# Kernel optimization log

Measured on AMD Instinct MI355X. Metric: run time of the kernel, lower is better.

## Reference

```python
import jax, jax.numpy as jnp
import numpy as np

KH, KW = 3, 3
STRIDE = (1, 1)


def setup_inputs() -> dict:
    key = jax.random.key(0)
    k1, k2, k3 = jax.random.split(key, 3)
    N, C, H, W = 16, 128, 64, 64
    O = 128
    x = jax.random.normal(k1, (N, C, H, W), dtype=jnp.float32)
    # Flat weight layout [O, C*KH*KW], matching torch reshape of [O,C,KH,KW]
    weight = jax.random.normal(k2, (O, C * KH * KW), dtype=jnp.float32) * 0.02
    bias = jax.random.normal(k3, (O, 1), dtype=jnp.float32) * 0.02
    return {"x": x, "weight": weight, "bias": bias}


def reference(x, weight, bias):
    O = weight.shape[0]
    C = x.shape[1]
    # [O, C*KH*KW] -> [O, C, KH, KW]; flattening order (C major, then kh, kw)
    # matches the module's unfold/permute im2col layout.
    w4 = weight.reshape(O, C, KH, KW)
    out = jax.lax.conv_general_dilated(
        x, w4,
        window_strides=STRIDE,
        padding='VALID',
        dimension_numbers=('NCHW', 'OIHW', 'NCHW'),
    )
    return out + bias.reshape(1, O, 1, 1)
```

## Files before the change

### kernel.cpp

```cpp
#include <hip/hip_runtime.h>
#include <stdint.h>

#define AS_G __attribute__((address_space(1)))
#define AS_L __attribute__((address_space(3)))

typedef __bf16 bf16x8 __attribute__((ext_vector_type(8)));
typedef float  f32x4  __attribute__((ext_vector_type(4)));

static constexpr int NIMG = 16, CIN = 128, H = 64, W = 64, OCH = 128;
static constexpr int HO = 62, WO = 62;
static constexpr int PIX = HO * WO;
static constexpr int M_TOT = NIMG * PIX;
static constexpr int K_TOT = CIN * 9;
static constexpr int BM = 64, BK = 64;
static constexpr int KSTEPS = K_TOT / BK;

__device__ __forceinline__ unsigned short f2bf(float f) {
    union { float f; uint32_t u; } v; v.f = f;
    uint32_t u = v.u;
    return (unsigned short)((u + 0x7FFFu + ((u >> 16) & 1u)) >> 16);
}

__global__ __launch_bounds__(256) void xpose_kernel(const float* __restrict__ x,
                                                    unsigned short* __restrict__ xt) {
    __shared__ float lds[CIN][W + 4];
    const int n   = blockIdx.x >> 6;
    const int h   = blockIdx.x & 63;
    const int tid = threadIdx.x;
    {
        const int c  = tid >> 1;
        const int w0 = (tid & 1) * 32;
        const float* src = x + (((size_t)(n * CIN + c) * H + h) * W + w0);
        #pragma unroll
        for (int j = 0; j < 8; ++j) {
            float4 v = *reinterpret_cast<const float4*>(src + j * 4);
            *reinterpret_cast<float4*>(&lds[c][w0 + j * 4]) = v;
        }
    }
    __syncthreads();
    {
        const int w  = tid >> 2;
        const int c0 = (tid & 3) * 32;
        unsigned short* dst = xt + (((size_t)(n * H + h) * W + w) * CIN + c0);
        uint32_t pk[16];
        #pragma unroll
        for (int j = 0; j < 16; ++j) {
            uint32_t lo = f2bf(lds[c0 + 2 * j][w]);
            uint32_t hi = f2bf(lds[c0 + 2 * j + 1][w]);
            pk[j] = lo | (hi << 16);
        }
        #pragma unroll
        for (int j = 0; j < 4; ++j) {
            *reinterpret_cast<uint4*>(dst + j * 8) =
                make_uint4(pk[4 * j], pk[4 * j + 1], pk[4 * j + 2], pk[4 * j + 3]);
        }
    }
}

__global__ __launch_bounds__(256) void wprep_kernel(const float* __restrict__ wsrc,
                                                    unsigned short* __restrict__ bpd) {
    int tid = blockIdx.x * 256 + threadIdx.x;
    if (tid >= OCH * K_TOT) return;
    int o  = tid / K_TOT;
    int kp = tid - o * K_TOT;
    int t  = kp >> 7;
    int c  = kp & 127;
    bpd[tid] = f2bf(wsrc[o * K_TOT + c * 9 + t]);
}

__global__ __launch_bounds__(256) void gemm_kernel(const unsigned short* __restrict__ xt,
                                                   const unsigned short* __restrict__ bp,
                                                   const float* __restrict__ bias,
                                                   float* __restrict__ out) {
    __shared__ alignas(16) unsigned short As[BM * BK];
    __shared__ alignas(16) unsigned short Bs[OCH * BK];
    const int tid  = threadIdx.x;
    const int wv   = tid >> 6;
    const int lane = tid & 63;
    const int m0   = blockIdx.x * BM;

    const int csel = ((lane & 7) ^ (lane >> 3)) * 8;
    int aBase[2], bBase[4];
    #pragma unroll
    for (int i = 0; i < 2; ++i) {
        int row = (wv * 2 + i) * 8 + (lane >> 3);
        int m = m0 + row;
        int n  = m / PIX;
        int r  = m - n * PIX;
        int y  = r / WO;
        int xx = r - y * WO;
        aBase[i] = ((n * H + y) * W + xx) * CIN;
    }
    #pragma unroll
    for (int i = 0; i < 4; ++i) {
        int row = (wv * 4 + i) * 8 + (lane >> 3);
        bBase[i] = row * K_TOT;
    }

    const int wr = wv >> 1, wc = wv & 1;
    const int lr = lane & 15, lq = lane >> 4;
    const int aRow = (wr * 32 + lr) * 128;
    const int bRow = (wc * 64 + lr) * 128;
    int colx[2];
    #pragma unroll
    for (int ks = 0; ks < 2; ++ks)
        colx[ks] = (ks * 64 + lq * 16) ^ ((lane & 7) << 4);

    f32x4 acc[2][4];
    #pragma unroll
    for (int a = 0; a < 2; ++a)
        #pragma unroll
        for (int b = 0; b < 4; ++b)
            acc[a][b] = (f32x4){0.f, 0.f, 0.f, 0.f};

    const char* AsB = (const char*)As;
    const char* BsB = (const char*)Bs;

    for (int step = 0; step < KSTEPS; ++step) {
        const int t  = step >> 1;
        const int c0 = (step & 1) * 64;
        const int tapoff = (t / 3) * (W * CIN) + (t % 3) * CIN + c0;
        const int kb = step * BK;
        #pragma unroll
        for (int i = 0; i < 2; ++i)
            __builtin_amdgcn_global_load_lds(
                (AS_G unsigned int*)(xt + aBase[i] + tapoff + csel),
                (AS_L unsigned int*)((char*)As + (wv * 2 + i) * 1024),
                16, 0, 0);
        #pragma unroll
        for (int i = 0; i < 4; ++i)
            __builtin_amdgcn_global_load_lds(
                (AS_G unsigned int*)(bp + bBase[i] + kb + csel),
                (AS_L unsigned int*)((char*)Bs + (wv * 4 + i) * 1024),
                16, 0, 0);
        __syncthreads();
        #pragma unroll
        for (int ks = 0; ks < 2; ++ks) {
            bf16x8 af[2], bfr[4];
            #pragma unroll
            for (int mi = 0; mi < 2; ++mi)
                af[mi] = *(const bf16x8*)(AsB + aRow + mi * 2048 + colx[ks]);
            #pragma unroll
            for (int ni = 0; ni < 4; ++ni)
                bfr[ni] = *(const bf16x8*)(BsB + bRow + ni * 2048 + colx[ks]);
            #pragma unroll
            for (int mi = 0; mi < 2; ++mi)
                #pragma unroll
                for (int ni = 0; ni < 4; ++ni)
                    acc[mi][ni] = __builtin_amdgcn_mfma_f32_16x16x32_bf16(
                        bfr[ni], af[mi], acc[mi][ni], 0, 0, 0);
        }
        __syncthreads();
    }

    f32x4 bv[4];
    #pragma unroll
    for (int ni = 0; ni < 4; ++ni)
        bv[ni] = *(const f32x4*)(bias + wc * 64 + ni * 16 + lq * 4);
    #pragma unroll
    for (int mi = 0; mi < 2; ++mi) {
        int m = m0 + wr * 32 + mi * 16 + lr;
        int n  = m / PIX;
        int r  = m - n * PIX;
        int y  = r / WO;
        int xx = r - y * WO;
        float* ob = out + (size_t)n * OCH * PIX + y * WO + xx;
        #pragma unroll
        for (int ni = 0; ni < 4; ++ni)
            #pragma unroll
            for (int j = 0; j < 4; ++j) {
                int o = wc * 64 + ni * 16 + lq * 4 + j;
                ob[(size_t)o * PIX] = acc[mi][ni][j] + bv[ni][j];
            }
    }
}

extern "C" void kernel_launch(void* const* d_in, const int* in_sizes, int n_in,
                              void* d_out, int out_size, void* d_ws, size_t ws_size,
                              hipStream_t stream) {
    const float* x    = (const float*)d_in[0];
    const float* wsrc = (const float*)d_in[1];
    const float* bias = (const float*)d_in[2];
    float* out = (float*)d_out;
    unsigned short* xt = (unsigned short*)d_ws;
    unsigned short* bp = xt + (size_t)NIMG * H * W * CIN;
    xpose_kernel<<<dim3(NIMG * H), dim3(256), 0, stream>>>(x, xt);
    wprep_kernel<<<dim3((OCH * K_TOT + 255) / 256), dim3(256), 0, stream>>>(wsrc, bp);
    gemm_kernel<<<dim3(M_TOT / BM), dim3(256), 0, stream>>>(xt, bp, bias, out);
}
```

Before: 46.40 us.

## Double-buffer GEMM LDS staging and merge input/weight prep kernels

The GEMM main loop now uses two LDS buffers and issues the global-to-LDS loads for the next K step before computing the current one, so load latency overlaps the MFMA work. It keeps one barrier per iteration instead of two. The transpose and weight-conversion kernels are merged into a single launch, removing one kernel launch. LDS usage per block doubles, which may lower occupancy.

```diff
diff --git a/kernel.cpp b/kernel.cpp
--- a/kernel.cpp
+++ b/kernel.cpp
@@ -14,6 +14,7 @@
 static constexpr int K_TOT = CIN * 9;
 static constexpr int BM = 64, BK = 64;
 static constexpr int KSTEPS = K_TOT / BK;
+static constexpr int BUFB = 24576;
 
 __device__ __forceinline__ unsigned short f2bf(float f) {
     union { float f; uint32_t u; } v; v.f = f;
@@ -21,59 +22,60 @@
     return (unsigned short)((u + 0x7FFFu + ((u >> 16) & 1u)) >> 16);
 }
 
-__global__ __launch_bounds__(256) void xpose_kernel(const float* __restrict__ x,
-                                                    unsigned short* __restrict__ xt) {
+__global__ __launch_bounds__(256) void prep_kernel(const float* __restrict__ x,
+                                                   const float* __restrict__ wsrc,
+                                                   unsigned short* __restrict__ xt,
+                                                   unsigned short* __restrict__ bpd) {
     __shared__ float lds[CIN][W + 4];
-    const int n   = blockIdx.x >> 6;
-    const int h   = blockIdx.x & 63;
-    const int tid = threadIdx.x;
-    {
-        const int c  = tid >> 1;
-        const int w0 = (tid & 1) * 32;
-        const float* src = x + (((size_t)(n * CIN + c) * H + h) * W + w0);
-        #pragma unroll
-        for (int j = 0; j < 8; ++j) {
-            float4 v = *reinterpret_cast<const float4*>(src + j * 4);
-            *reinterpret_cast<float4*>(&lds[c][w0 + j * 4]) = v;
+    if (blockIdx.x < NIMG * H) {
+        const int n   = blockIdx.x >> 6;
+        const int h   = blockIdx.x & 63;
+        const int tid = threadIdx.x;
+        {
+            const int c  = tid >> 1;
+            const int w0 = (tid & 1) * 32;
+            const float* src = x + (((size_t)(n * CIN + c) * H + h) * W + w0);
+            #pragma unroll
+            for (int j = 0; j < 8; ++j) {
+                float4 v = *reinterpret_cast<const float4*>(src + j * 4);
+                *reinterpret_cast<float4*>(&lds[c][w0 + j * 4]) = v;
+            }
+        }
+        __syncthreads();
+        {
+            const int w  = tid >> 2;
+            const int c0 = (tid & 3) * 32;
+            unsigned short* dst = xt + (((size_t)(n * H + h) * W + w) * CIN + c0);
+            uint32_t pk[16];
+            #pragma unroll
+            for (int j = 0; j < 16; ++j) {
+                uint32_t lo = f2bf(lds[c0 + 2 * j][w]);
+                uint32_t hi = f2bf(lds[c0 + 2 * j + 1][w]);
+                pk[j] = lo | (hi << 16);
+            }
+            #pragma unroll
+            for (int j = 0; j < 4; ++j) {
+                *reinterpret_cast<uint4*>(dst + j * 8) =
+                    make_uint4(pk[4 * j], pk[4 * j + 1], pk[4 * j + 2], pk[4 * j + 3]);
+            }
+        }
+    } else {
+        int tid = (blockIdx.x - NIMG * H) * 256 + threadIdx.x;
+        if (tid < OCH * K_TOT) {
+            int o  = tid / K_TOT;
+            int kp = tid - o * K_TOT;
+            int t  = kp >> 7;
+            int c  = kp & 127;
+            bpd[tid] = f2bf(wsrc[o * K_TOT + c * 9 + t]);
         }
     }
-    __syncthreads();
-    {
-        const int w  = tid >> 2;
-        const int c0 = (tid & 3) * 32;
-        unsigned short* dst = xt + (((size_t)(n * H + h) * W + w) * CIN + c0);
-        uint32_t pk[16];
-        #pragma unroll
-        for (int j = 0; j < 16; ++j) {
-            uint32_t lo = f2bf(lds[c0 + 2 * j][w]);
-            uint32_t hi = f2bf(lds[c0 + 2 * j + 1][w]);
-            pk[j] = lo | (hi << 16);
-        }
-        #pragma unroll
-        for (int j = 0; j < 4; ++j) {
-            *reinterpret_cast<uint4*>(dst + j * 8) =
-                make_uint4(pk[4 * j], pk[4 * j + 1], pk[4 * j + 2], pk[4 * j + 3]);
-        }
-    }
-}
-
-__global__ __launch_bounds__(256) void wprep_kernel(const float* __restrict__ wsrc,
-                                                    unsigned short* __restrict__ bpd) {
-    int tid = blockIdx.x * 256 + threadIdx.x;
-    if (tid >= OCH * K_TOT) return;
-    int o  = tid / K_TOT;
-    int kp = tid - o * K_TOT;
-    int t  = kp >> 7;
-    int c  = kp & 127;
-    bpd[tid] = f2bf(wsrc[o * K_TOT + c * 9 + t]);
 }
 
 __global__ __launch_bounds__(256) void gemm_kernel(const unsigned short* __restrict__ xt,
                                                    const unsigned short* __restrict__ bp,
                                                    const float* __restrict__ bias,
                                                    float* __restrict__ out) {
-    __shared__ alignas(16) unsigned short As[BM * BK];
-    __shared__ alignas(16) unsigned short Bs[OCH * BK];
+    __shared__ alignas(16) char lds[2 * BUFB];
     const int tid  = threadIdx.x;
     const int wv   = tid >> 6;
     const int lane = tid & 63;
@@ -92,10 +94,26 @@
         aBase[i] = ((n * H + y) * W + xx) * CIN;
     }
     #pragma unroll
-    for (int i = 0; i < 4; ++i) {
-        int row = (wv * 4 + i) * 8 + (lane >> 3);
-        bBase[i] = row * K_TOT;
-    }
+    for (int i = 0; i < 4; ++i)
+        bBase[i] = ((wv * 4 + i) * 8 + (lane >> 3)) * K_TOT;
+
+    auto stage = [&](int buf, int step) {
+        const int t  = step >> 1;
+        const int c0 = (step & 1) * 64;
+        const int tapoff = (t / 3) * (W * CIN) + (t % 3) * CIN + c0;
+        const int kb = step * BK;
+        char* dst = lds + buf * BUFB;
+        #pragma unroll
+        for (int i = 0; i < 2; ++i)
+            __builtin_amdgcn_global_load_lds(
+                (AS_G unsigned int*)(xt + aBase[i] + tapoff + csel),
+                (AS_L unsigned int*)(dst + (wv * 2 + i) * 1024), 16, 0, 0);
+        #pragma unroll
+        for (int i = 0; i < 4; ++i)
+            __builtin_amdgcn_global_load_lds(
+                (AS_G unsigned int*)(bp + bBase[i] + kb + csel),
+                (AS_L unsigned int*)(dst + 8192 + (wv * 4 + i) * 1024), 16, 0, 0);
+    };
 
     const int wr = wv >> 1, wc = wv & 1;
     const int lr = lane & 15, lq = lane >> 4;
@@ -113,36 +131,23 @@
         for (int b = 0; b < 4; ++b)
             acc[a][b] = (f32x4){0.f, 0.f, 0.f, 0.f};
 
-    const char* AsB = (const char*)As;
-    const char* BsB = (const char*)Bs;
+    stage(0, 0);
+    __syncthreads();
 
+    #pragma unroll 2
     for (int step = 0; step < KSTEPS; ++step) {
-        const int t  = step >> 1;
-        const int c0 = (step & 1) * 64;
-        const int tapoff = (t / 3) * (W * CIN) + (t % 3) * CIN + c0;
-        const int kb = step * BK;
-        #pragma unroll
-        for (int i = 0; i < 2; ++i)
-            __builtin_amdgcn_global_load_lds(
-                (AS_G unsigned int*)(xt + aBase[i] + tapoff + csel),
-                (AS_L unsigned int*)((char*)As + (wv * 2 + i) * 1024),
-                16, 0, 0);
-        #pragma unroll
-        for (int i = 0; i < 4; ++i)
-            __builtin_amdgcn_global_load_lds(
-                (AS_G unsigned int*)(bp + bBase[i] + kb + csel),
-                (AS_L unsigned int*)((char*)Bs + (wv * 4 + i) * 1024),
-                16, 0, 0);
-        __syncthreads();
+        const int buf = step & 1;
+        if (step + 1 < KSTEPS) stage(buf ^ 1, step + 1);
+        const char* base = lds + buf * BUFB;
         #pragma unroll
         for (int ks = 0; ks < 2; ++ks) {
             bf16x8 af[2], bfr[4];
             #pragma unroll
             for (int mi = 0; mi < 2; ++mi)
-                af[mi] = *(const bf16x8*)(AsB + aRow + mi * 2048 + colx[ks]);
+                af[mi] = *(const bf16x8*)(base + aRow + mi * 2048 + colx[ks]);
             #pragma unroll
             for (int ni = 0; ni < 4; ++ni)
-                bfr[ni] = *(const bf16x8*)(BsB + bRow + ni * 2048 + colx[ks]);
+                bfr[ni] = *(const bf16x8*)(base + 8192 + bRow + ni * 2048 + colx[ks]);
             #pragma unroll
             for (int mi = 0; mi < 2; ++mi)
                 #pragma unroll
@@ -184,7 +189,7 @@
     float* out = (float*)d_out;
     unsigned short* xt = (unsigned short*)d_ws;
     unsigned short* bp = xt + (size_t)NIMG * H * W * CIN;
-    xpose_kernel<<<dim3(NIMG * H), dim3(256), 0, stream>>>(x, xt);
-    wprep_kernel<<<dim3((OCH * K_TOT + 255) / 256), dim3(256), 0, stream>>>(wsrc, bp);
+    prep_kernel<<<dim3(NIMG * H + (OCH * K_TOT + 255) / 256), dim3(256), 0, stream>>>(
+        x, wsrc, xt, bp);
     gemm_kernel<<<dim3(M_TOT / BM), dim3(256), 0, stream>>>(xt, bp, bias, out);
 }
```

Measured after the change: 48.72 us. 5.0% more time.

## Merge prep kernels and remap GEMM workgroups to contiguous XCD chunks

Applied to the files above, without the earlier changes.

Fuses the input-transpose and weight-prep kernels into one launch, with blocks split by block index, to save a kernel launch and its gap. In the GEMM, blockIdx is remapped so that each of the 8 XCDs (blocks are assigned round-robin) handles a contiguous range of M tiles: 121 tiles for the first XCD and 120 for each of the others. The aim is L2 reuse of the overlapping 3x3 input rows between neighbouring tiles on the same XCD. The remap hardcodes the tile count and assumes round-robin XCD dispatch.

```diff
diff --git a/kernel.cpp b/kernel.cpp
--- a/kernel.cpp
+++ b/kernel.cpp
@@ -14,6 +14,7 @@
 static constexpr int K_TOT = CIN * 9;
 static constexpr int BM = 64, BK = 64;
 static constexpr int KSTEPS = K_TOT / BK;
+static constexpr int NWG = M_TOT / BM;
 
 __device__ __forceinline__ unsigned short f2bf(float f) {
     union { float f; uint32_t u; } v; v.f = f;
@@ -21,51 +22,53 @@
     return (unsigned short)((u + 0x7FFFu + ((u >> 16) & 1u)) >> 16);
 }
 
-__global__ __launch_bounds__(256) void xpose_kernel(const float* __restrict__ x,
-                                                    unsigned short* __restrict__ xt) {
+__global__ __launch_bounds__(256) void prep_kernel(const float* __restrict__ x,
+                                                   const float* __restrict__ wsrc,
+                                                   unsigned short* __restrict__ xt,
+                                                   unsigned short* __restrict__ bpd) {
     __shared__ float lds[CIN][W + 4];
-    const int n   = blockIdx.x >> 6;
-    const int h   = blockIdx.x & 63;
-    const int tid = threadIdx.x;
-    {
-        const int c  = tid >> 1;
-        const int w0 = (tid & 1) * 32;
-        const float* src = x + (((size_t)(n * CIN + c) * H + h) * W + w0);
-        #pragma unroll
-        for (int j = 0; j < 8; ++j) {
-            float4 v = *reinterpret_cast<const float4*>(src + j * 4);
-            *reinterpret_cast<float4*>(&lds[c][w0 + j * 4]) = v;
+    if (blockIdx.x < NIMG * H) {
+        const int n   = blockIdx.x >> 6;
+        const int h   = blockIdx.x & 63;
+        const int tid = threadIdx.x;
+        {
+            const int c  = tid >> 1;
+            const int w0 = (tid & 1) * 32;
+            const float* src = x + (((size_t)(n * CIN + c) * H + h) * W + w0);
+            #pragma unroll
+            for (int j = 0; j < 8; ++j) {
+                float4 v = *reinterpret_cast<const float4*>(src + j * 4);
+                *reinterpret_cast<float4*>(&lds[c][w0 + j * 4]) = v;
+            }
+        }
+        __syncthreads();
+        {
+            const int w  = tid >> 2;
+            const int c0 = (tid & 3) * 32;
+            unsigned short* dst = xt + (((size_t)(n * H + h) * W + w) * CIN + c0);
+            uint32_t pk[16];
+            #pragma unroll
+            for (int j = 0; j < 16; ++j) {
+                uint32_t lo = f2bf(lds[c0 + 2 * j][w]);
+                uint32_t hi = f2bf(lds[c0 + 2 * j + 1][w]);
+                pk[j] = lo | (hi << 16);
+            }
+            #pragma unroll
+            for (int j = 0; j < 4; ++j) {
+                *reinterpret_cast<uint4*>(dst + j * 8) =
+                    make_uint4(pk[4 * j], pk[4 * j + 1], pk[4 * j + 2], pk[4 * j + 3]);
+            }
+        }
+    } else {
+        int tid = (blockIdx.x - NIMG * H) * 256 + threadIdx.x;
+        if (tid < OCH * K_TOT) {
+            int o  = tid / K_TOT;
+            int kp = tid - o * K_TOT;
+            int t  = kp >> 7;
+            int c  = kp & 127;
+            bpd[tid] = f2bf(wsrc[o * K_TOT + c * 9 + t]);
         }
     }
-    __syncthreads();
-    {
-        const int w  = tid >> 2;
-        const int c0 = (tid & 3) * 32;
-        unsigned short* dst = xt + (((size_t)(n * H + h) * W + w) * CIN + c0);
-        uint32_t pk[16];
-        #pragma unroll
-        for (int j = 0; j < 16; ++j) {
-            uint32_t lo = f2bf(lds[c0 + 2 * j][w]);
-            uint32_t hi = f2bf(lds[c0 + 2 * j + 1][w]);
-            pk[j] = lo | (hi << 16);
-        }
-        #pragma unroll
-        for (int j = 0; j < 4; ++j) {
-            *reinterpret_cast<uint4*>(dst + j * 8) =
-                make_uint4(pk[4 * j], pk[4 * j + 1], pk[4 * j + 2], pk[4 * j + 3]);
-        }
-    }
-}
-
-__global__ __launch_bounds__(256) void wprep_kernel(const float* __restrict__ wsrc,
-                                                    unsigned short* __restrict__ bpd) {
-    int tid = blockIdx.x * 256 + threadIdx.x;
-    if (tid >= OCH * K_TOT) return;
-    int o  = tid / K_TOT;
-    int kp = tid - o * K_TOT;
-    int t  = kp >> 7;
-    int c  = kp & 127;
-    bpd[tid] = f2bf(wsrc[o * K_TOT + c * 9 + t]);
 }
 
 __global__ __launch_bounds__(256) void gemm_kernel(const unsigned short* __restrict__ xt,
@@ -77,7 +80,12 @@
     const int tid  = threadIdx.x;
     const int wv   = tid >> 6;
     const int lane = tid & 63;
-    const int m0   = blockIdx.x * BM;
+
+    const int orig = blockIdx.x;
+    const int xcd  = orig & 7;
+    const int idx  = orig >> 3;
+    const int wg   = (xcd == 0 ? 0 : 121 + (xcd - 1) * 120) + idx;
+    const int m0   = wg * BM;
 
     const int csel = ((lane & 7) ^ (lane >> 3)) * 8;
     int aBase[2], bBase[4];
@@ -92,10 +100,8 @@
         aBase[i] = ((n * H + y) * W + xx) * CIN;
     }
     #pragma unroll
-    for (int i = 0; i < 4; ++i) {
-        int row = (wv * 4 + i) * 8 + (lane >> 3);
-        bBase[i] = row * K_TOT;
-    }
+    for (int i = 0; i < 4; ++i)
+        bBase[i] = ((wv * 4 + i) * 8 + (lane >> 3)) * K_TOT;
 
     const int wr = wv >> 1, wc = wv & 1;
     const int lr = lane & 15, lq = lane >> 4;
@@ -184,7 +190,7 @@
     float* out = (float*)d_out;
     unsigned short* xt = (unsigned short*)d_ws;
     unsigned short* bp = xt + (size_t)NIMG * H * W * CIN;
-    xpose_kernel<<<dim3(NIMG * H), dim3(256), 0, stream>>>(x, xt);
-    wprep_kernel<<<dim3((OCH * K_TOT + 255) / 256), dim3(256), 0, stream>>>(wsrc, bp);
-    gemm_kernel<<<dim3(M_TOT / BM), dim3(256), 0, stream>>>(xt, bp, bias, out);
+    prep_kernel<<<dim3(NIMG * H + (OCH * K_TOT + 255) / 256), dim3(256), 0, stream>>>(
+        x, wsrc, xt, bp);
+    gemm_kernel<<<dim3(NWG), dim3(256), 0, stream>>>(xt, bp, bias, out);
 }
```

New measurement: 43.53 us. 6.2% less time.
